# Optimization experiments

Hardware: AMD Instinct MI355X
Metric: run time of the kernel (lower is better)

The kernel has to match this reference:

```python
import jax, jax.numpy as jnp
import numpy as np

B = 32; NPG = 500; N = B * NPG; E = 256000; F = 1024; OD = 128
DD = 80; TD = 32; NH = 4; DH = TD // NH; DFF = 128; NL = 2
LSUB = 128; MAXLEN = 4 * LSUB
NEG = -1e9; SLOPE = 0.01; EPS = 1e-5


def setup_inputs() -> dict:
    key = jax.random.key(0)
    ks = iter(jax.random.split(key, 64))
    nrm = lambda *s: jax.random.normal(next(ks), s, jnp.float32)
    w = lambda *s: nrm(*s) * 0.02
    inp = {}
    inp["pro1_x"] = nrm(N, F)
    inp["pro2_x"] = nrm(N, F)
    inp["pro1_edge_index"] = jax.random.randint(next(ks), (2, E), 0, N)
    inp["pro2_edge_index"] = jax.random.randint(next(ks), (2, E), 0, N)
    inp["pro1_batch"] = jnp.repeat(jnp.arange(B), NPG)
    inp["pro2_batch"] = jnp.repeat(jnp.arange(B), NPG)
    for nm in ("mas1_straight", "mas1_flipped", "mas2_straight", "mas2_flipped"):
        inp[nm] = nrm(B, LSUB, DD)
        inp[nm + "_lengths"] = jax.random.randint(next(ks), (B,), 1, LSUB + 1)
    inp["gcn1_w"] = w(F, F); inp["gcn1_b"] = jnp.zeros(F)
    inp["gcn2_w"] = w(F, F); inp["gcn2_b"] = jnp.zeros(F)
    inp["fc1_w"] = w(OD, F); inp["fc1_b"] = jnp.zeros(OD)
    inp["fc2_w"] = w(OD, F); inp["fc2_b"] = jnp.zeros(OD)
    inp["red_w"] = w(TD - 2, DD); inp["red_b"] = jnp.zeros(TD - 2)
    inp["attn_in_w"] = w(NL, 3 * TD, TD); inp["attn_in_b"] = jnp.zeros((NL, 3 * TD))
    inp["attn_out_w"] = w(NL, TD, TD); inp["attn_out_b"] = jnp.zeros((NL, TD))
    inp["ln1_w"] = jnp.ones((NL, TD)); inp["ln1_b"] = jnp.zeros((NL, TD))
    inp["ln2_w"] = jnp.ones((NL, TD)); inp["ln2_b"] = jnp.zeros((NL, TD))
    inp["ff1_w"] = w(NL, DFF, TD); inp["ff1_b"] = jnp.zeros((NL, DFF))
    inp["ff2_w"] = w(NL, TD, DFF); inp["ff2_b"] = jnp.zeros((NL, TD))
    inp["final_w"] = w(1, 2 * OD + TD); inp["final_b"] = jnp.zeros(1)
    return inp


def _leaky(v):
    return jnp.where(v >= 0, v, SLOPE * v)


def _gcn(x, ei, W, b):
    # GCNConv: x' = D^-1/2 (A + I) D^-1/2 (x @ W^T) + b
    sl = jnp.arange(N, dtype=ei.dtype)
    src = jnp.concatenate([ei[0], sl])
    dst = jnp.concatenate([ei[1], sl])
    deg = jax.ops.segment_sum(jnp.ones(src.shape[0], x.dtype), dst, N)
    dinv = jax.lax.rsqrt(deg)
    norm = (dinv[src] * dinv[dst])[:, None]
    h = x @ W.T
    return jax.ops.segment_sum(h[src] * norm, dst, N) + b


def _gmp(x, batch):
    # global mean pool per graph
    s = jax.ops.segment_sum(x, batch, B)
    c = jax.ops.segment_sum(jnp.ones(x.shape[0], x.dtype), batch, B)
    return s / c[:, None]


def _ln(x, w, b):
    m = x.mean(-1, keepdims=True)
    v = ((x - m) ** 2).mean(-1, keepdims=True)
    return (x - m) * jax.lax.rsqrt(v + EPS) * w + b


def _forward(pro1_x, pro1_edge_index, pro1_batch, pro2_x, pro2_edge_index, pro2_batch,
             mas1_straight, mas1_flipped, mas2_straight, mas2_flipped,
             mas1_straight_lengths, mas1_flipped_lengths, mas2_straight_lengths, mas2_flipped_lengths,
             gcn1_w, gcn1_b, fc1_w, fc1_b, gcn2_w, gcn2_b, fc2_w, fc2_b,
             red_w, red_b, attn_in_w, attn_in_b, attn_out_w, attn_out_b,
             ln1_w, ln1_b, ln2_w, ln2_b, ff1_w, ff1_b, ff2_w, ff2_b,
             final_w, final_b):
    # --- graph branches (dropout = identity at inference) ---
    x1 = _leaky(_gcn(pro1_x, pro1_edge_index, gcn1_w, gcn1_b))
    x1 = _leaky(_gmp(x1, pro1_batch) @ fc1_w.T + fc1_b)           # [B, OD]
    x2 = _leaky(_gcn(pro2_x, pro2_edge_index, gcn2_w, gcn2_b))
    x2 = _leaky(_gmp(x2, pro2_batch) @ fc2_w.T + fc2_b)           # [B, OD]

    # --- vectorized ragged pack: project, append indicators, scatter to offsets ---
    inds = ((1.0, 1.0), (0.0, 1.0), (1.0, 0.0), (0.0, 0.0))      # (straight, first)
    mas = (mas1_straight, mas1_flipped, mas2_straight, mas2_flipped)
    lens = (mas1_straight_lengths, mas1_flipped_lengths, mas2_straight_lengths, mas2_flipped_lengths)
    pos = jnp.arange(LSUB)
    brow = jnp.arange(B)[:, None]
    seq = jnp.zeros((B, MAXLEN, TD), jnp.float32)
    off = jnp.zeros((B,), lens[0].dtype)
    for m, l, (si, fi) in zip(mas, lens, inds):
        proj = m @ red_w.T + red_b                                # [B, LSUB, TD-2]
        ones = jnp.ones((B, LSUB, 1), jnp.float32)
        p = jnp.concatenate([proj, si * ones, fi * ones], -1)    # [B, LSUB, TD]
        valid = pos[None, :] < l[:, None]                        # [B, LSUB]
        idx = jnp.where(valid, off[:, None] + pos[None, :], 0)
        seq = seq.at[brow, idx].add(p * valid[..., None])
        off = off + l
    mask = jnp.arange(MAXLEN)[None, :] < off[:, None]            # [B, MAXLEN] True = valid

    # --- post-norm TransformerEncoder (relu FFN, key padding mask) ---
    x_t = seq
    for li in range(NL):
        qkv = x_t @ attn_in_w[li].T + attn_in_b[li]
        q, k, v = jnp.split(qkv, 3, axis=-1)
        q = q.reshape(B, MAXLEN, NH, DH)
        k = k.reshape(B, MAXLEN, NH, DH)
        v = v.reshape(B, MAXLEN, NH, DH)
        scores = jnp.einsum('bqhd,bkhd->bhqk', q, k) / np.float32(np.sqrt(DH))
        scores = jnp.where(mask[:, None, None, :], scores, NEG)
        attn = jax.nn.softmax(scores, axis=-1)
        o = jnp.einsum('bhqk,bkhd->bqhd', attn, v).reshape(B, MAXLEN, TD)
        o = o @ attn_out_w[li].T + attn_out_b[li]
        x_t = _ln(x_t + o, ln1_w[li], ln1_b[li])
        h = jax.nn.relu(x_t @ ff1_w[li].T + ff1_b[li]) @ ff2_w[li].T + ff2_b[li]
        x_t = _ln(x_t + h, ln2_w[li], ln2_b[li])

    mf = mask[..., None].astype(jnp.float32)
    mas_out = (x_t * mf).sum(1) / mf.sum(1)                      # masked mean [B, TD]

    combined = jnp.concatenate([x1, x2, mas_out], axis=1)        # [B, 2*OD + TD]
    return combined @ final_w.T + final_b                        # [B, 1]


def reference(pro1_x, pro1_edge_index, pro1_batch, pro2_x, pro2_edge_index, pro2_batch,
              mas1_straight, mas1_flipped, mas2_straight, mas2_flipped,
              mas1_straight_lengths, mas1_flipped_lengths, mas2_straight_lengths, mas2_flipped_lengths,
              gcn1_w, gcn1_b, fc1_w, fc1_b, gcn2_w, gcn2_b, fc2_w, fc2_b,
              red_w, red_b, attn_in_w, attn_in_b, attn_out_w, attn_out_b,
              ln1_w, ln1_b, ln2_w, ln2_b, ff1_w, ff1_b, ff2_w, ff2_b,
              final_w, final_b):
    return _forward(pro1_x, pro1_edge_index, pro1_batch, pro2_x, pro2_edge_index, pro2_batch,
                    mas1_straight, mas1_flipped, mas2_straight, mas2_flipped,
                    mas1_straight_lengths, mas1_flipped_lengths, mas2_straight_lengths, mas2_flipped_lengths,
                    gcn1_w, gcn1_b, fc1_w, fc1_b, gcn2_w, gcn2_b, fc2_w, fc2_b,
                    red_w, red_b, attn_in_w, attn_in_b, attn_out_w, attn_out_b,
                    ln1_w, ln1_b, ln2_w, ln2_b, ff1_w, ff1_b, ff2_w, ff2_b,
                    final_w, final_b)
```

## Files before the change

### kernel.cpp

```cpp
#include <hip/hip_runtime.h>
#include <stdint.h>

#define N_NODES 16000
#define MPAD_   16128
#define B_      32
#define NPG_    500
#define E_      256000
#define F_      1024
#define OD_     128
#define DD_     80
#define TD_     32
#define NH_     4
#define DH_     8
#define DFF_    128
#define LSUB_   128
#define MAXLEN_ 512
#define EPS_    1e-5f
#define SLOPE_  0.01f

typedef __bf16 bf16x8 __attribute__((ext_vector_type(8)));
typedef float  f32x4  __attribute__((ext_vector_type(4)));

__device__ __forceinline__ float leaky(float v) { return v >= 0.f ? v : SLOPE_ * v; }

__device__ __forceinline__ unsigned short f2bf(float f) {
  unsigned u = __float_as_uint(f);
  u += 0x7FFFu + ((u >> 16) & 1u);
  return (unsigned short)(u >> 16);
}
__device__ __forceinline__ float bf2f(unsigned short u) {
  return __uint_as_float((unsigned)u << 16);
}

__device__ __forceinline__ void gld_lds16(const void* g, void* l) {
  __builtin_amdgcn_global_load_lds(
      (const __attribute__((address_space(1))) unsigned int*)g,
      (__attribute__((address_space(3))) unsigned int*)l, 16, 0, 0);
}

__global__ void k_f2bf2(const float* __restrict__ in0, const float* __restrict__ in1,
                        unsigned short* __restrict__ out0, unsigned short* __restrict__ out1,
                        int n4) {
  const float* in = blockIdx.y ? in1 : in0;
  unsigned short* out = blockIdx.y ? out1 : out0;
  int i = blockIdx.x * blockDim.x + threadIdx.x;
  int stride = gridDim.x * blockDim.x;
  for (; i < n4; i += stride) {
    float4 v = ((const float4*)in)[i];
    ushort4 o;
    o.x = f2bf(v.x); o.y = f2bf(v.y); o.z = f2bf(v.z); o.w = f2bf(v.w);
    ((ushort4*)out)[i] = o;
  }
}

#define LDSA(bf, ks, row) (*(const bf16x8*)&lds[(bf)*16384 + (ks)*8192 + (row)*32 + rs])
#define LDSB(bf, ks, row) (*(const bf16x8*)&lds[32768 + (bf)*16384 + (ks)*8192 + (row)*32 + rs])
#define STG_A(bf, R, kti) do { \
  gld_lds16(&Ag[(size_t)(mBase + (R) + r4) * 1024 + (kti) * 64 + c4],      &lds[(bf)*16384 + (R)*32 + t*8]); \
  gld_lds16(&Ag[(size_t)(mBase + (R) + r4) * 1024 + (kti) * 64 + 32 + c4], &lds[(bf)*16384 + 8192 + (R)*32 + t*8]); \
} while (0)
#define STG_B(bf, R, kti) do { \
  gld_lds16(&Bg[(size_t)(nBase + (R) + r4) * 1024 + (kti) * 64 + c4],      &lds[32768 + (bf)*16384 + (R)*32 + t*8]); \
  gld_lds16(&Bg[(size_t)(nBase + (R) + r4) * 1024 + (kti) * 64 + 32 + c4], &lds[32768 + (bf)*16384 + 8192 + (R)*32 + t*8]); \
} while (0)
#define RD_Q0(bf) do { \
  _Pragma("unroll") for (int mi = 0; mi < 4; ++mi) \
  _Pragma("unroll") for (int ks = 0; ks < 2; ++ks) \
    aLo[mi][ks] = LDSA(bf, ks, wrow * 128 + mi * 16 + l15); \
  _Pragma("unroll") for (int ni = 0; ni < 2; ++ni) \
  _Pragma("unroll") for (int ks = 0; ks < 2; ++ks) \
    bLo[ni][ks] = LDSB(bf, ks, wcol * 64 + ni * 16 + l15); \
} while (0)
#define RD_BHI(bf) do { \
  _Pragma("unroll") for (int ni = 0; ni < 2; ++ni) \
  _Pragma("unroll") for (int ks = 0; ks < 2; ++ks) \
    bHi[ni][ks] = LDSB(bf, ks, wcol * 64 + (2 + ni) * 16 + l15); \
} while (0)
#define RD_AHI(bf) do { \
  _Pragma("unroll") for (int mi = 0; mi < 4; ++mi) \
  _Pragma("unroll") for (int ks = 0; ks < 2; ++ks) \
    aHi[mi][ks] = LDSA(bf, ks, wrow * 128 + (4 + mi) * 16 + l15); \
} while (0)
#define MM_Q0() do { __builtin_amdgcn_s_setprio(1); \
  _Pragma("unroll") for (int mi = 0; mi < 4; ++mi) \
  _Pragma("unroll") for (int ni = 0; ni < 2; ++ni) \
  _Pragma("unroll") for (int ks = 0; ks < 2; ++ks) \
    acc[mi][ni] = __builtin_amdgcn_mfma_f32_16x16x32_bf16(aLo[mi][ks], bLo[ni][ks], acc[mi][ni], 0, 0, 0); \
  __builtin_amdgcn_s_setprio(0); } while (0)
#define MM_Q1() do { __builtin_amdgcn_s_setprio(1); \
  _Pragma("unroll") for (int mi = 0; mi < 4; ++mi) \
  _Pragma("unroll") for (int ni = 0; ni < 2; ++ni) \
  _Pragma("unroll") for (int ks = 0; ks < 2; ++ks) \
    acc[mi][2 + ni] = __builtin_amdgcn_mfma_f32_16x16x32_bf16(aLo[mi][ks], bHi[ni][ks], acc[mi][2 + ni], 0, 0, 0); \
  __builtin_amdgcn_s_setprio(0); } while (0)
#define MM_Q3() do { __builtin_amdgcn_s_setprio(1); \
  _Pragma("unroll") for (int mi = 0; mi < 4; ++mi) \
  _Pragma("unroll") for (int ni = 0; ni < 2; ++ni) \
  _Pragma("unroll") for (int ks = 0; ks < 2; ++ks) \
    acc[4 + mi][2 + ni] = __builtin_amdgcn_mfma_f32_16x16x32_bf16(aHi[mi][ks], bHi[ni][ks], acc[4 + mi][2 + ni], 0, 0, 0); \
  __builtin_amdgcn_s_setprio(0); } while (0)
#define MM_Q2() do { __builtin_amdgcn_s_setprio(1); \
  _Pragma("unroll") for (int mi = 0; mi < 4; ++mi) \
  _Pragma("unroll") for (int ni = 0; ni < 2; ++ni) \
  _Pragma("unroll") for (int ks = 0; ks < 2; ++ks) \
    acc[4 + mi][ni] = __builtin_amdgcn_mfma_f32_16x16x32_bf16(aHi[mi][ks], bLo[ni][ks], acc[4 + mi][ni], 0, 0, 0); \
  __builtin_amdgcn_s_setprio(0); } while (0)
#define BAR() do { __builtin_amdgcn_sched_barrier(0); __builtin_amdgcn_s_barrier(); \
                   __builtin_amdgcn_sched_barrier(0); } while (0)
#define LGKM0() do { asm volatile("s_waitcnt lgkmcnt(0)" ::: "memory"); \
                     __builtin_amdgcn_sched_barrier(0); } while (0)
#define VM4() do { asm volatile("s_waitcnt vmcnt(4)" ::: "memory"); } while (0)
#define VM0() do { asm volatile("s_waitcnt vmcnt(0)" ::: "memory"); } while (0)

__global__ __launch_bounds__(512, 2) void k_gemm256(const unsigned short* __restrict__ Ag,
                                                    const unsigned short* __restrict__ Bg,
                                                    unsigned short* __restrict__ Cg) {
  __shared__ short lds[65536];
  const int j  = blockIdx.x;
  const int x8 = j & 7;
  const int chunk = (x8 < 4) ? x8 * 32 : 128 + (x8 - 4) * 31;
  const int pos = chunk + (j >> 3);
  const int mb = pos >> 2, nb = pos & 3;
  const size_t g = blockIdx.z;
  Ag += g * (size_t)MPAD_ * 1024;
  Bg += g * (size_t)1024 * 1024;
  Cg += g * (size_t)MPAD_ * 1024;
  const int t = threadIdx.x;
  const int lane = t & 63, wave = t >> 6;
  const int wrow = wave >> 2, wcol = wave & 3;
  const int quad = lane >> 4, l15 = lane & 15;
  const int mBase = mb * 256, nBase = nb * 256;
  const int r4 = t >> 2;
  const int c4 = (((t & 3) - ((t >> 3) & 3)) & 3) * 8;
  const int rs = ((quad + (l15 >> 1)) & 3) * 8;

  f32x4 acc[8][4];
  f32x4 zero = {0.f, 0.f, 0.f, 0.f};
#pragma unroll
  for (int i = 0; i < 8; ++i)
#pragma unroll
    for (int jn = 0; jn < 4; ++jn) acc[i][jn] = zero;

  bf16x8 aLo[4][2], aHi[4][2], bLo[2][2], bHi[2][2];

  STG_A(0, 0, 0); STG_A(0, 128, 0); STG_B(0, 0, 0); STG_B(0, 128, 0);
  STG_B(1, 0, 1); STG_B(1, 128, 1);
  VM4();
  BAR();

  for (int kt = 0; kt < 16; kt += 2) {
    const bool s2 = (kt + 2) < 16;
    const bool s3 = (kt + 3) < 16;
    RD_Q0(0);
    STG_A(1, 0, kt + 1);
    BAR(); LGKM0(); MM_Q0(); BAR();
    RD_BHI(0);
    STG_A(1, 128, kt + 1);
    BAR(); LGKM0(); MM_Q1(); BAR();
    RD_AHI(0);
    if (s2) STG_B(0, 0, kt + 2);
    BAR(); LGKM0(); MM_Q3(); BAR();
    if (s2) { STG_B(0, 128, kt + 2); VM4(); } else VM0();
    BAR(); MM_Q2(); BAR();
    RD_Q0(1);
    if (s2) STG_A(0, 0, kt + 2);
    BAR(); LGKM0(); MM_Q0(); BAR();
    RD_BHI(1);
    if (s2) STG_A(0, 128, kt + 2);
    BAR(); LGKM0(); MM_Q1(); BAR();
    RD_AHI(1);
    if (s3) STG_B(1, 0, kt + 3);
    BAR(); LGKM0(); MM_Q3(); BAR();
    if (s3) { STG_B(1, 128, kt + 3); VM4(); }
    BAR(); MM_Q2(); BAR();
  }

#pragma unroll
  for (int mi = 0; mi < 8; ++mi)
#pragma unroll
    for (int ni = 0; ni < 4; ++ni)
#pragma unroll
      for (int r = 0; r < 4; ++r) {
        int grow = mBase + wrow * 128 + mi * 16 + quad * 4 + r;
        int gcol = nBase + wcol * 64 + ni * 16 + l15;
        Cg[(size_t)grow * 1024 + gcol] = f2bf(acc[mi][ni][r]);
      }
}

__global__ void k_hist(const int* __restrict__ ei0, const int* __restrict__ ei1,
                       int* __restrict__ cnt, int e, int n) {
  const int g = blockIdx.y;
  const int* dst = (g ? ei1 : ei0) + e;
  int i = blockIdx.x * 256 + threadIdx.x;
  if (i < e) atomicAdd(&cnt[g * n + dst[i]], 1);
}

__global__ void k_scan(const int* __restrict__ cnt_all, int* __restrict__ rowstart_all,
                       int* __restrict__ cursor_all, float* __restrict__ dinv_all, int n) {
  const int g = blockIdx.x;
  const int* cnt = cnt_all + g * n;
  int* rowstart = rowstart_all + g * (n + 1);
  int* cursor   = cursor_all + g * n;
  float* dinv   = dinv_all + g * n;
  __shared__ int part[256];
  __shared__ int base[257];
  int t = threadIdx.x;
  int chunk = (n + 255) >> 8;
  int s = 0;
  for (int j = 0; j < chunk; ++j) {
    int idx = t * chunk + j;
    if (idx < n) s += cnt[idx];
  }
  part[t] = s;
  __syncthreads();
  if (t == 0) {
    int a = 0;
    for (int i = 0; i < 256; ++i) { base[i] = a; a += part[i]; }
    base[256] = a;
  }
  __syncthreads();
  int a = base[t];
  for (int j = 0; j < chunk; ++j) {
    int idx = t * chunk + j;
    if (idx < n) {
      int c = cnt[idx];
      rowstart[idx] = a; cursor[idx] = a; a += c;
      dinv[idx] = rsqrtf((float)c + 1.0f);
    }
  }
  if (t == 0) rowstart[n] = base[256];
}

__global__ void k_scatter(const int* __restrict__ ei0, const int* __restrict__ ei1,
                          const float* __restrict__ dinv_all, int* __restrict__ cursor_all,
                          int* __restrict__ csr_all, float* __restrict__ csrw_all,
                          int e, int n) {
  const int g = blockIdx.y;
  const int* ei = g ? ei1 : ei0;
  int i = blockIdx.x * 256 + threadIdx.x;
  if (i < e) {
    int s = ei[i], d = ei[e + i];
    int p = atomicAdd(&cursor_all[g * n + d], 1);
    csr_all[(size_t)g * e + p]  = s;
    csrw_all[(size_t)g * e + p] = dinv_all[g * n + s] * dinv_all[g * n + d];
  }
}

__global__ __launch_bounds__(64) void k_gather(const ushort2* __restrict__ h2,
                                               const float* __restrict__ dinv,
                                               const int* __restrict__ rowstart,
                                               const int* __restrict__ csr,
                                               const float* __restrict__ csrw,
                                               ushort2* __restrict__ agg2) {
  const int sl = blockIdx.x;
  const int i  = blockIdx.y;
  const int t  = threadIdx.x;
  __shared__ int   ssrc[64];
  __shared__ float sw[64];
  const float di = dinv[i];
  const size_t fo = (size_t)sl * 64 + t;
  ushort2 sv = h2[(size_t)i * 512 + fo];
  const float selfw = di * di;
  float ax = bf2f(sv.x) * selfw, ay = bf2f(sv.y) * selfw;
  const int beg = rowstart[i], end = rowstart[i + 1];
  for (int base = beg; base < end; base += 64) {
    int c = end - base; if (c > 64) c = 64;
    __syncthreads();
    if (t < c) { ssrc[t] = csr[base + t]; sw[t] = csrw[base + t]; }
    __syncthreads();
    int j = 0;
    for (; j + 4 <= c; j += 4) {
      ushort2 v0 = h2[(size_t)ssrc[j]     * 512 + fo];
      ushort2 v1 = h2[(size_t)ssrc[j + 1] * 512 + fo];
      ushort2 v2 = h2[(size_t)ssrc[j + 2] * 512 + fo];
      ushort2 v3 = h2[(size_t)ssrc[j + 3] * 512 + fo];
      float w0 = sw[j], w1 = sw[j + 1], w2 = sw[j + 2], w3 = sw[j + 3];
      ax += bf2f(v0.x) * w0 + bf2f(v1.x) * w1 + bf2f(v2.x) * w2 + bf2f(v3.x) * w3;
      ay += bf2f(v0.y) * w0 + bf2f(v1.y) * w1 + bf2f(v2.y) * w2 + bf2f(v3.y) * w3;
    }
    for (; j < c; ++j) {
      ushort2 v0 = h2[(size_t)ssrc[j] * 512 + fo];
      float w0 = sw[j];
      ax += bf2f(v0.x) * w0; ay += bf2f(v0.y) * w0;
    }
  }
  ushort2 o; o.x = f2bf(ax); o.y = f2bf(ay);
  agg2[(size_t)i * 512 + fo] = o;
}

__global__ void k_pool(const unsigned short* __restrict__ agg_all,
                       const float* __restrict__ bias0, const float* __restrict__ bias1,
                       float* __restrict__ pooled_all) {
  int f = blockIdx.x * 256 + threadIdx.x;
  int z = blockIdx.z;
  int g = z >> 5, b = z & 31;
  const unsigned short* agg = agg_all + (size_t)g * N_NODES * F_;
  const float* bias = g ? bias1 : bias0;
  float* pooled = pooled_all + (size_t)g * B_ * F_;
  int r0 = blockIdx.y * 100;
  float bf = bias[f];
  float s = 0.f;
  for (int r = 0; r < 100; ++r)
    s += leaky(bf2f(agg[(size_t)(b * NPG_ + r0 + r) * F_ + f]) + bf);
  atomicAdd(&pooled[b * F_ + f], s);
}

__global__ void k_fc(const float* __restrict__ pooled_all,
                     const float* __restrict__ w0, const float* __restrict__ w1,
                     const float* __restrict__ bias0, const float* __restrict__ bias1,
                     float* __restrict__ out0, float* __restrict__ out1) {
  int b = blockIdx.x, o = threadIdx.x, g = blockIdx.y;
  const float* p  = pooled_all + (size_t)g * B_ * F_ + b * F_;
  const float* wr = (g ? w1 : w0) + o * F_;
  const float* bias = g ? bias1 : bias0;
  float* out = g ? out1 : out0;
  float acc = 0.f;
  for (int f = 0; f < F_; ++f) acc += p[f] * wr[f];
  out[b * OD_ + o] = leaky(acc * (1.f / 500.f) + bias[o]);
}

__global__ void k_pack(const float* __restrict__ m0, const float* __restrict__ m1,
                       const float* __restrict__ m2, const float* __restrict__ m3,
                       const int* __restrict__ l0, const int* __restrict__ l1,
                       const int* __restrict__ l2, const int* __restrict__ l3,
                       const float* __restrict__ rw, const float* __restrict__ rb,
                       float* __restrict__ seq) {
  __shared__ float xs[DD_];
  const int p = blockIdx.x, b = blockIdx.y, k = blockIdx.z;
  const float* mas = (k == 0) ? m0 : (k == 1) ? m1 : (k == 2) ? m2 : m3;
  const int*   lk  = (k == 0) ? l0 : (k == 1) ? l1 : (k == 2) ? l2 : l3;
  const int len = lk[b];
  if (p >= len) return;
  int off = 0;
  if (k > 0) off += l0[b];
  if (k > 1) off += l1[b];
  if (k > 2) off += l2[b];
  const int t = threadIdx.x;
  for (int d = t; d < DD_; d += 64) xs[d] = mas[(size_t)(b * LSUB_ + p) * DD_ + d];
  __syncthreads();
  if (t < TD_) {
    float v;
    if (t < TD_ - 2) {
      float a = rb[t];
      const float* w = &rw[t * DD_];
      for (int d = 0; d < DD_; ++d) a += xs[d] * w[d];
      v = a;
    } else if (t == TD_ - 2) {
      v = (k == 0 || k == 2) ? 1.f : 0.f;
    } else {
      v = (k < 2) ? 1.f : 0.f;
    }
    seq[((size_t)b * MAXLEN_ + off + p) * TD_ + t] = v;
  }
}

__global__ void k_totlen(const int* __restrict__ l0, const int* __restrict__ l1,
                         const int* __restrict__ l2, const int* __restrict__ l3,
                         int* __restrict__ tot) {
  int b = threadIdx.x;
  if (b < B_) tot[b] = l0[b] + l1[b] + l2[b] + l3[b];
}

__global__ void k_qkv(const float* __restrict__ xt, const float* __restrict__ w,
                      const float* __restrict__ bias, const int* __restrict__ tot,
                      float* __restrict__ qkv) {
  __shared__ float xs[TD_];
  const int row = blockIdx.x;
  if ((row & (MAXLEN_ - 1)) >= tot[row >> 9]) return;
  const int t = threadIdx.x;
  if (t < TD_) xs[t] = xt[(size_t)row * TD_ + t];
  __syncthreads();
  if (t < 3 * TD_) {
    float a = bias[t];
    const float* wr = &w[t * TD_];
#pragma unroll
    for (int k = 0; k < TD_; ++k) a += xs[k] * wr[k];
    qkv[(size_t)row * 96 + t] = a;
  }
}

__global__ __launch_bounds__(128) void k_attn(const float* __restrict__ qkv,
                                              const int* __restrict__ tot,
                                              float* __restrict__ obuf) {
  __shared__ float Kl[MAXLEN_ * DH_];
  __shared__ float Vl[MAXLEN_ * DH_];
  const int h = blockIdx.x, b = blockIdx.y, qz = blockIdx.z;
  const int t = threadIdx.x;
  const int L = tot[b];
  if (qz * 64 >= L) return;
  const float* base = &qkv[(size_t)b * MAXLEN_ * 96];
  for (int i = t; i < L * DH_; i += 128) {
    int p = i >> 3, d = i & 7;
    Kl[i] = base[p * 96 + 32 + h * 8 + d];
    Vl[i] = base[p * 96 + 64 + h * 8 + d];
  }
  __syncthreads();
  const int qi = qz * 64 + (t >> 1);
  if (qi >= L) return;
  const int half = t & 1;
  const float scale = 0.35355339059327373f;
  float q[8];
#pragma unroll
  for (int d = 0; d < 8; ++d) q[d] = base[qi * 96 + h * 8 + d] * scale;

  float l0 = 0.f, l1 = 0.f;
  float a0[8] = {0, 0, 0, 0, 0, 0, 0, 0};
  float a1[8] = {0, 0, 0, 0, 0, 0, 0, 0};
  int j = half;
  for (; j + 2 < L; j += 4) {
    const float* kr0 = &Kl[j * 8];
    const float* kr1 = &Kl[(j + 2) * 8];
    float s0 = 0.f, s1 = 0.f;
#pragma unroll
    for (int d = 0; d < 8; ++d) { s0 += q[d] * kr0[d]; s1 += q[d] * kr1[d]; }
    float p0 = __expf(s0), p1 = __expf(s1);
    l0 += p0; l1 += p1;
    const float* vr0 = &Vl[j * 8];
    const float* vr1 = &Vl[(j + 2) * 8];
#pragma unroll
    for (int d = 0; d < 8; ++d) { a0[d] += p0 * vr0[d]; a1[d] += p1 * vr1[d]; }
  }
  for (; j < L; j += 2) {
    const float* kr = &Kl[j * 8];
    float s = 0.f;
#pragma unroll
    for (int d = 0; d < 8; ++d) s += q[d] * kr[d];
    float p = __expf(s);
    l0 += p;
    const float* vr = &Vl[j * 8];
#pragma unroll
    for (int d = 0; d < 8; ++d) a0[d] += p * vr[d];
  }
  float l = l0 + l1;
#pragma unroll
  for (int d = 0; d < 8; ++d) a0[d] += a1[d];
  l += __shfl_xor(l, 1);
#pragma unroll
  for (int d = 0; d < 8; ++d) a0[d] += __shfl_xor(a0[d], 1);
  float inv = 1.f / l;
  const int dbase = half * 4;
  float4 o;
  o.x = a0[dbase + 0] * inv; o.y = a0[dbase + 1] * inv;
  o.z = a0[dbase + 2] * inv; o.w = a0[dbase + 3] * inv;
  *(float4*)&obuf[((size_t)b * MAXLEN_ + qi) * TD_ + h * 8 + dbase] = o;
}

__global__ void k_oproj_ln(const float* __restrict__ obuf, const float* __restrict__ w,
                           const float* __restrict__ bias, const float* __restrict__ lw,
                           const float* __restrict__ lb, const int* __restrict__ tot,
                           float* __restrict__ xt) {
  const int t = threadIdx.x;
  const int r = blockIdx.x * 8 + (t >> 5);
  if ((r & (MAXLEN_ - 1)) >= tot[r >> 9]) return;
  const int j = t & 31;
  const float* orow = &obuf[(size_t)r * TD_];
  float a = bias[j] + xt[(size_t)r * TD_ + j];
  const float* wr = &w[j * TD_];
#pragma unroll
  for (int k = 0; k < TD_; ++k) a += orow[k] * wr[k];
  float s1 = a, s2 = a * a;
#pragma unroll
  for (int m = 1; m < 32; m <<= 1) {
    s1 += __shfl_xor(s1, m, 32);
    s2 += __shfl_xor(s2, m, 32);
  }
  float mean = s1 * (1.f / 32.f);
  float var  = s2 * (1.f / 32.f) - mean * mean;
  xt[(size_t)r * TD_ + j] = (a - mean) * rsqrtf(var + EPS_) * lw[j] + lb[j];
}

__global__ void k_ffn_ln(const float* __restrict__ w1, const float* __restrict__ b1,
                         const float* __restrict__ w2, const float* __restrict__ b2,
                         const float* __restrict__ lw, const float* __restrict__ lb,
                         const int* __restrict__ tot, float* __restrict__ xt) {
  const int r = blockIdx.x, t = threadIdx.x;
  if ((r & (MAXLEN_ - 1)) >= tot[r >> 9]) return;
  __shared__ float xs[TD_];
  __shared__ float hb[DFF_];
  if (t < TD_) xs[t] = xt[(size_t)r * TD_ + t];
  __syncthreads();
  {
    float a = b1[t];
    const float* wr = &w1[t * TD_];
#pragma unroll
    for (int k = 0; k < TD_; ++k) a += xs[k] * wr[k];
    hb[t] = fmaxf(a, 0.f);
  }
  __syncthreads();
  if (t < TD_) {
    float a = b2[t] + xs[t];
    const float* wr = &w2[t * DFF_];
#pragma unroll
    for (int k = 0; k < DFF_; ++k) a += hb[k] * wr[k];
    float s1 = a, s2 = a * a;
#pragma unroll
    for (int m = 1; m < 32; m <<= 1) {
      s1 += __shfl_xor(s1, m, 32);
      s2 += __shfl_xor(s2, m, 32);
    }
    float mean = s1 * (1.f / 32.f);
    float var  = s2 * (1.f / 32.f) - mean * mean;
    xt[(size_t)r * TD_ + t] = (a - mean) * rsqrtf(var + EPS_) * lw[t] + lb[t];
  }
}

__global__ void k_maskmean(const float* __restrict__ xt, const int* __restrict__ tot,
                           float* __restrict__ mout) {
  __shared__ float sbuf[8][32];
  const int b = blockIdx.x, t = threadIdx.x;
  const int j = t & 31, c = t >> 5;
  const int L = tot[b];
  float s = 0.f;
  for (int p = c; p < L; p += 8) s += xt[((size_t)b * MAXLEN_ + p) * TD_ + j];
  sbuf[c][j] = s;
  __syncthreads();
  if (t < 32) {
    float a = 0.f;
#pragma unroll
    for (int cc = 0; cc < 8; ++cc) a += sbuf[cc][t];
    mout[b * TD_ + t] = a / (float)L;
  }
}

__global__ void k_final(const float* __restrict__ x1, const float* __restrict__ x2,
                        const float* __restrict__ mo, const float* __restrict__ fw,
                        const float* __restrict__ fb, float* __restrict__ out) {
  const int b = blockIdx.x, t = threadIdx.x;
  float s = 0.f;
  for (int i = t; i < 2 * OD_ + TD_; i += 64) {
    float c = (i < OD_) ? x1[b * OD_ + i]
            : (i < 2 * OD_) ? x2[b * OD_ + (i - OD_)]
            : mo[b * TD_ + (i - 2 * OD_)];
    s += fw[i] * c;
  }
#pragma unroll
  for (int m = 1; m < 64; m <<= 1) s += __shfl_xor(s, m, 64);
  if (t == 0) out[b] = s + fb[0];
}

extern "C" void kernel_launch(void* const* d_in, const int* in_sizes, int n_in,
                              void* d_out, int out_size, void* d_ws, size_t ws_size,
                              hipStream_t stream) {
  (void)in_sizes; (void)n_in; (void)out_size; (void)ws_size;
  const float* pro_x[2]  = {(const float*)d_in[0], (const float*)d_in[1]};
  const int*   pro_ei[2] = {(const int*)d_in[2], (const int*)d_in[3]};
  const float* mas[4]    = {(const float*)d_in[6], (const float*)d_in[8],
                            (const float*)d_in[10], (const float*)d_in[12]};
  const int*   lens[4]   = {(const int*)d_in[7], (const int*)d_in[9],
                            (const int*)d_in[11], (const int*)d_in[13]};
  const float* gw[2]  = {(const float*)d_in[14], (const float*)d_in[16]};
  const float* gb[2]  = {(const float*)d_in[15], (const float*)d_in[17]};
  const float* fcw[2] = {(const float*)d_in[18], (const float*)d_in[20]};
  const float* fcb[2] = {(const float*)d_in[19], (const float*)d_in[21]};
  const float* red_w = (const float*)d_in[22];
  const float* red_b = (const float*)d_in[23];
  const float* attn_in_w  = (const float*)d_in[24];
  const float* attn_in_b  = (const float*)d_in[25];
  const float* attn_out_w = (const float*)d_in[26];
  const float* attn_out_b = (const float*)d_in[27];
  const float* ln1_w = (const float*)d_in[28];
  const float* ln1_b = (const float*)d_in[29];
  const float* ln2_w = (const float*)d_in[30];
  const float* ln2_b = (const float*)d_in[31];
  const float* ff1_w = (const float*)d_in[32];
  const float* ff1_b = (const float*)d_in[33];
  const float* ff2_w = (const float*)d_in[34];
  const float* ff2_b = (const float*)d_in[35];
  const float* final_w = (const float*)d_in[36];
  const float* final_b = (const float*)d_in[37];
  float* out = (float*)d_out;

  char* p = (char*)d_ws;
  auto carve = [&](size_t bytes) -> void* {
    void* r = (void*)p;
    p += (bytes + 255) & ~(size_t)255;
    return r;
  };
  unsigned short* xb  = (unsigned short*)carve((size_t)2 * MPAD_ * F_ * 2);
  unsigned short* Wb  = (unsigned short*)carve((size_t)2 * F_ * F_ * 2);
  unsigned short* h   = (unsigned short*)carve((size_t)2 * MPAD_ * F_ * 2);
  unsigned short* agg = (unsigned short*)carve((size_t)2 * N_NODES * F_ * 2);
  int*   cnt      = (int*)carve((size_t)2 * N_NODES * 4);
  float* dinv     = (float*)carve((size_t)2 * N_NODES * 4);
  int*   rowstart = (int*)carve((size_t)2 * (N_NODES + 1) * 4);
  int*   cursor   = (int*)carve((size_t)2 * N_NODES * 4);
  int*   csr      = (int*)carve((size_t)2 * E_ * 4);
  float* csrw     = (float*)carve((size_t)2 * E_ * 4);
  float* pooled   = (float*)carve((size_t)2 * B_ * F_ * 4);
  float* xg[2];
  xg[0] = (float*)carve((size_t)B_ * OD_ * 4);
  xg[1] = (float*)carve((size_t)B_ * OD_ * 4);
  float* seq    = (float*)carve((size_t)B_ * MAXLEN_ * TD_ * 4);
  float* qkv    = (float*)carve((size_t)B_ * MAXLEN_ * 96 * 4);
  float* obuf   = (float*)carve((size_t)B_ * MAXLEN_ * TD_ * 4);
  int*   totlen = (int*)carve((size_t)B_ * 4);
  float* masout = (float*)carve((size_t)B_ * TD_ * 4);

  k_f2bf2<<<dim3(1024, 2), 256, 0, stream>>>(pro_x[0], pro_x[1], xb,
                                             xb + (size_t)MPAD_ * F_, (N_NODES * F_) / 4);
  k_f2bf2<<<dim3(512, 2), 256, 0, stream>>>(gw[0], gw[1], Wb, Wb + (size_t)F_ * F_,
                                            (F_ * F_) / 4);
  k_gemm256<<<dim3(252, 1, 2), 512, 0, stream>>>(xb, Wb, h);
  hipMemsetAsync(cnt, 0, (size_t)2 * N_NODES * 4, stream);
  k_hist<<<dim3(1000, 2), 256, 0, stream>>>(pro_ei[0], pro_ei[1], cnt, E_, N_NODES);
  k_scan<<<2, 256, 0, stream>>>(cnt, rowstart, cursor, dinv, N_NODES);
  k_scatter<<<dim3(1000, 2), 256, 0, stream>>>(pro_ei[0], pro_ei[1], dinv, cursor,
                                               csr, csrw, E_, N_NODES);
  for (int g = 0; g < 2; ++g) {
    k_gather<<<dim3(8, N_NODES), 64, 0, stream>>>(
        (const ushort2*)(h + (size_t)g * MPAD_ * F_), dinv + (size_t)g * N_NODES,
        rowstart + (size_t)g * (N_NODES + 1), csr + (size_t)g * E_, csrw + (size_t)g * E_,
        (ushort2*)(agg + (size_t)g * N_NODES * F_));
  }
  hipMemsetAsync(pooled, 0, (size_t)2 * B_ * F_ * 4, stream);
  k_pool<<<dim3(4, 5, 64), 256, 0, stream>>>(agg, gb[0], gb[1], pooled);
  k_fc<<<dim3(B_, 2), 128, 0, stream>>>(pooled, fcw[0], fcw[1], fcb[0], fcb[1],
                                        xg[0], xg[1]);

  hipMemsetAsync(seq, 0, (size_t)B_ * MAXLEN_ * TD_ * 4, stream);
  k_pack<<<dim3(LSUB_, B_, 4), 64, 0, stream>>>(mas[0], mas[1], mas[2], mas[3],
                                                lens[0], lens[1], lens[2], lens[3],
                                                red_w, red_b, seq);
  k_totlen<<<1, 64, 0, stream>>>(lens[0], lens[1], lens[2], lens[3], totlen);

  for (int li = 0; li < 2; ++li) {
    k_qkv<<<B_ * MAXLEN_, 128, 0, stream>>>(seq, attn_in_w + (size_t)li * 96 * TD_,
                                            attn_in_b + (size_t)li * 96, totlen, qkv);
    k_attn<<<dim3(NH_, B_, 8), 128, 0, stream>>>(qkv, totlen, obuf);
    k_oproj_ln<<<(B_ * MAXLEN_) / 8, 256, 0, stream>>>(
        obuf, attn_out_w + (size_t)li * TD_ * TD_, attn_out_b + (size_t)li * TD_,
        ln1_w + (size_t)li * TD_, ln1_b + (size_t)li * TD_, totlen, seq);
    k_ffn_ln<<<B_ * MAXLEN_, 128, 0, stream>>>(
        ff1_w + (size_t)li * DFF_ * TD_, ff1_b + (size_t)li * DFF_,
        ff2_w + (size_t)li * TD_ * DFF_, ff2_b + (size_t)li * TD_,
        ln2_w + (size_t)li * TD_, ln2_b + (size_t)li * TD_, totlen, seq);
  }

  k_maskmean<<<B_, 256, 0, stream>>>(seq, totlen, masout);
  k_final<<<B_, 64, 0, stream>>>(xg[0], xg[1], masout, final_w, final_b, out);
}
```

Measured before the change: 782.9 us.

## Merge GCN gathers, fuse post-attention and final kernels, coalesce FC

The two per-graph edge-gather launches become one grid with four nodes per block. Each wave now reads CSR indices and weights straight from global memory instead of staging them in shared memory behind barriers. The FC kernel caches the pooled row in shared memory, and each wave computes output rows with coalesced weight reads and a shuffle reduction. The out-projection+LayerNorm and FFN+LayerNorm kernels are fused into one per-row kernel, mask-mean and the final dot product are fused, and the memset of the sequence buffer is dropped. This cuts launches, barriers and intermediate memory round trips, but it relies on padded sequence rows never being read uninitialised.

```diff
diff --git a/kernel.cpp b/kernel.cpp
--- a/kernel.cpp
+++ b/kernel.cpp
@@ -246,43 +246,44 @@
   }
 }
 
-__global__ __launch_bounds__(64) void k_gather(const ushort2* __restrict__ h2,
-                                               const float* __restrict__ dinv,
-                                               const int* __restrict__ rowstart,
-                                               const int* __restrict__ csr,
-                                               const float* __restrict__ csrw,
-                                               ushort2* __restrict__ agg2) {
+__global__ __launch_bounds__(256) void k_gather(const ushort2* __restrict__ h2_all,
+                                                const float* __restrict__ dinv_all,
+                                                const int* __restrict__ rowstart_all,
+                                                const int* __restrict__ csr_all,
+                                                const float* __restrict__ csrw_all,
+                                                ushort2* __restrict__ agg2_all) {
+  const int g = blockIdx.z;
+  const ushort2* h2 = h2_all + (size_t)g * MPAD_ * 512;
+  const float* dinv = dinv_all + (size_t)g * N_NODES;
+  const int* rowstart = rowstart_all + (size_t)g * (N_NODES + 1);
+  const int* csr = csr_all + (size_t)g * E_;
+  const float* csrw = csrw_all + (size_t)g * E_;
+  ushort2* agg2 = agg2_all + (size_t)g * N_NODES * 512;
   const int sl = blockIdx.x;
-  const int i  = blockIdx.y;
-  const int t  = threadIdx.x;
-  __shared__ int   ssrc[64];
-  __shared__ float sw[64];
+  const int i  = blockIdx.y * 4 + (threadIdx.x >> 6);
+  const int lane = threadIdx.x & 63;
+  const size_t fo = (size_t)sl * 64 + lane;
   const float di = dinv[i];
-  const size_t fo = (size_t)sl * 64 + t;
   ushort2 sv = h2[(size_t)i * 512 + fo];
   const float selfw = di * di;
   float ax = bf2f(sv.x) * selfw, ay = bf2f(sv.y) * selfw;
   const int beg = rowstart[i], end = rowstart[i + 1];
-  for (int base = beg; base < end; base += 64) {
-    int c = end - base; if (c > 64) c = 64;
-    __syncthreads();
-    if (t < c) { ssrc[t] = csr[base + t]; sw[t] = csrw[base + t]; }
-    __syncthreads();
-    int j = 0;
-    for (; j + 4 <= c; j += 4) {
-      ushort2 v0 = h2[(size_t)ssrc[j]     * 512 + fo];
-      ushort2 v1 = h2[(size_t)ssrc[j + 1] * 512 + fo];
-      ushort2 v2 = h2[(size_t)ssrc[j + 2] * 512 + fo];
-      ushort2 v3 = h2[(size_t)ssrc[j + 3] * 512 + fo];
-      float w0 = sw[j], w1 = sw[j + 1], w2 = sw[j + 2], w3 = sw[j + 3];
-      ax += bf2f(v0.x) * w0 + bf2f(v1.x) * w1 + bf2f(v2.x) * w2 + bf2f(v3.x) * w3;
-      ay += bf2f(v0.y) * w0 + bf2f(v1.y) * w1 + bf2f(v2.y) * w2 + bf2f(v3.y) * w3;
-    }
-    for (; j < c; ++j) {
-      ushort2 v0 = h2[(size_t)ssrc[j] * 512 + fo];
-      float w0 = sw[j];
-      ax += bf2f(v0.x) * w0; ay += bf2f(v0.y) * w0;
-    }
+  int j = beg;
+  for (; j + 4 <= end; j += 4) {
+    int s0 = csr[j], s1 = csr[j + 1], s2 = csr[j + 2], s3 = csr[j + 3];
+    float w0 = csrw[j], w1 = csrw[j + 1], w2 = csrw[j + 2], w3 = csrw[j + 3];
+    ushort2 v0 = h2[(size_t)s0 * 512 + fo];
+    ushort2 v1 = h2[(size_t)s1 * 512 + fo];
+    ushort2 v2 = h2[(size_t)s2 * 512 + fo];
+    ushort2 v3 = h2[(size_t)s3 * 512 + fo];
+    ax += bf2f(v0.x) * w0 + bf2f(v1.x) * w1 + bf2f(v2.x) * w2 + bf2f(v3.x) * w3;
+    ay += bf2f(v0.y) * w0 + bf2f(v1.y) * w1 + bf2f(v2.y) * w2 + bf2f(v3.y) * w3;
+  }
+  for (; j < end; ++j) {
+    int s0 = csr[j];
+    float w0 = csrw[j];
+    ushort2 v0 = h2[(size_t)s0 * 512 + fo];
+    ax += bf2f(v0.x) * w0; ay += bf2f(v0.y) * w0;
   }
   ushort2 o; o.x = f2bf(ax); o.y = f2bf(ay);
   agg2[(size_t)i * 512 + fo] = o;
@@ -305,18 +306,29 @@
   atomicAdd(&pooled[b * F_ + f], s);
 }
 
-__global__ void k_fc(const float* __restrict__ pooled_all,
+__global__ __launch_bounds__(256) void k_fc(const float* __restrict__ pooled_all,
                      const float* __restrict__ w0, const float* __restrict__ w1,
                      const float* __restrict__ bias0, const float* __restrict__ bias1,
                      float* __restrict__ out0, float* __restrict__ out1) {
-  int b = blockIdx.x, o = threadIdx.x, g = blockIdx.y;
-  const float* p  = pooled_all + (size_t)g * B_ * F_ + b * F_;
-  const float* wr = (g ? w1 : w0) + o * F_;
+  __shared__ float ps[F_];
+  const int b = blockIdx.x, g = blockIdx.y, t = threadIdx.x;
+  const float* p = pooled_all + (size_t)g * B_ * F_ + b * F_;
+  const float* w = g ? w1 : w0;
   const float* bias = g ? bias1 : bias0;
   float* out = g ? out1 : out0;
-  float acc = 0.f;
-  for (int f = 0; f < F_; ++f) acc += p[f] * wr[f];
-  out[b * OD_ + o] = leaky(acc * (1.f / 500.f) + bias[o]);
+  ((float4*)ps)[t] = ((const float4*)p)[t];
+  __syncthreads();
+  const int wave = t >> 6, lane = t & 63;
+  for (int oo = 0; oo < 32; ++oo) {
+    const int o = wave * 32 + oo;
+    const float* wr = w + (size_t)o * F_;
+    float a = 0.f;
+#pragma unroll
+    for (int c = 0; c < 16; ++c) a += wr[c * 64 + lane] * ps[c * 64 + lane];
+#pragma unroll
+    for (int m = 1; m < 64; m <<= 1) a += __shfl_xor(a, m, 64);
+    if (lane == 0) out[b * OD_ + o] = leaky(a * (1.f / 500.f) + bias[o]);
+  }
 }
 
 __global__ void k_pack(const float* __restrict__ m0, const float* __restrict__ m1,
@@ -445,53 +457,29 @@
   *(float4*)&obuf[((size_t)b * MAXLEN_ + qi) * TD_ + h * 8 + dbase] = o;
 }
 
-__global__ void k_oproj_ln(const float* __restrict__ obuf, const float* __restrict__ w,
-                           const float* __restrict__ bias, const float* __restrict__ lw,
-                           const float* __restrict__ lb, const int* __restrict__ tot,
-                           float* __restrict__ xt) {
-  const int t = threadIdx.x;
-  const int r = blockIdx.x * 8 + (t >> 5);
-  if ((r & (MAXLEN_ - 1)) >= tot[r >> 9]) return;
-  const int j = t & 31;
-  const float* orow = &obuf[(size_t)r * TD_];
-  float a = bias[j] + xt[(size_t)r * TD_ + j];
-  const float* wr = &w[j * TD_];
-#pragma unroll
-  for (int k = 0; k < TD_; ++k) a += orow[k] * wr[k];
-  float s1 = a, s2 = a * a;
-#pragma unroll
-  for (int m = 1; m < 32; m <<= 1) {
-    s1 += __shfl_xor(s1, m, 32);
-    s2 += __shfl_xor(s2, m, 32);
-  }
-  float mean = s1 * (1.f / 32.f);
-  float var  = s2 * (1.f / 32.f) - mean * mean;
-  xt[(size_t)r * TD_ + j] = (a - mean) * rsqrtf(var + EPS_) * lw[j] + lb[j];
-}
-
-__global__ void k_ffn_ln(const float* __restrict__ w1, const float* __restrict__ b1,
-                         const float* __restrict__ w2, const float* __restrict__ b2,
-                         const float* __restrict__ lw, const float* __restrict__ lb,
-                         const int* __restrict__ tot, float* __restrict__ xt) {
+__global__ __launch_bounds__(128) void k_post(const float* __restrict__ obuf,
+                                              const float* __restrict__ ow,
+                                              const float* __restrict__ ob,
+                                              const float* __restrict__ l1w,
+                                              const float* __restrict__ l1b,
+                                              const float* __restrict__ f1w,
+                                              const float* __restrict__ f1b,
+                                              const float* __restrict__ f2w,
+                                              const float* __restrict__ f2b,
+                                              const float* __restrict__ l2w,
+                                              const float* __restrict__ l2b,
+                                              const int* __restrict__ tot,
+                                              float* __restrict__ xt) {
   const int r = blockIdx.x, t = threadIdx.x;
   if ((r & (MAXLEN_ - 1)) >= tot[r >> 9]) return;
   __shared__ float xs[TD_];
   __shared__ float hb[DFF_];
-  if (t < TD_) xs[t] = xt[(size_t)r * TD_ + t];
-  __syncthreads();
-  {
-    float a = b1[t];
-    const float* wr = &w1[t * TD_];
-#pragma unroll
-    for (int k = 0; k < TD_; ++k) a += xs[k] * wr[k];
-    hb[t] = fmaxf(a, 0.f);
-  }
-  __syncthreads();
   if (t < TD_) {
-    float a = b2[t] + xs[t];
-    const float* wr = &w2[t * DFF_];
-#pragma unroll
-    for (int k = 0; k < DFF_; ++k) a += hb[k] * wr[k];
+    const float* orow = &obuf[(size_t)r * TD_];
+    float a = ob[t] + xt[(size_t)r * TD_ + t];
+    const float* wr = &ow[t * TD_];
+#pragma unroll
+    for (int k = 0; k < TD_; ++k) a += orow[k] * wr[k];
     float s1 = a, s2 = a * a;
 #pragma unroll
     for (int m = 1; m < 32; m <<= 1) {
@@ -500,13 +488,43 @@
     }
     float mean = s1 * (1.f / 32.f);
     float var  = s2 * (1.f / 32.f) - mean * mean;
-    xt[(size_t)r * TD_ + t] = (a - mean) * rsqrtf(var + EPS_) * lw[t] + lb[t];
-  }
-}
-
-__global__ void k_maskmean(const float* __restrict__ xt, const int* __restrict__ tot,
-                           float* __restrict__ mout) {
+    xs[t] = (a - mean) * rsqrtf(var + EPS_) * l1w[t] + l1b[t];
+  }
+  __syncthreads();
+  {
+    float a = f1b[t];
+    const float* wr = &f1w[t * TD_];
+#pragma unroll
+    for (int k = 0; k < TD_; ++k) a += xs[k] * wr[k];
+    hb[t] = fmaxf(a, 0.f);
+  }
+  __syncthreads();
+  if (t < TD_) {
+    float a = f2b[t] + xs[t];
+    const float* wr = &f2w[t * DFF_];
+#pragma unroll
+    for (int k = 0; k < DFF_; ++k) a += hb[k] * wr[k];
+    float s1 = a, s2 = a * a;
+#pragma unroll
+    for (int m = 1; m < 32; m <<= 1) {
+      s1 += __shfl_xor(s1, m, 32);
+      s2 += __shfl_xor(s2, m, 32);
+    }
+    float mean = s1 * (1.f / 32.f);
+    float var  = s2 * (1.f / 32.f) - mean * mean;
+    xt[(size_t)r * TD_ + t] = (a - mean) * rsqrtf(var + EPS_) * l2w[t] + l2b[t];
+  }
+}
+
+__global__ __launch_bounds__(256) void k_maskfinal(const float* __restrict__ xt,
+                                                   const int* __restrict__ tot,
+                                                   const float* __restrict__ x1,
+                                                   const float* __restrict__ x2,
+                                                   const float* __restrict__ fw,
+                                                   const float* __restrict__ fb,
+                                                   float* __restrict__ out) {
   __shared__ float sbuf[8][32];
+  __shared__ float mo[TD_];
   const int b = blockIdx.x, t = threadIdx.x;
   const int j = t & 31, c = t >> 5;
   const int L = tot[b];
@@ -518,24 +536,21 @@
     float a = 0.f;
 #pragma unroll
     for (int cc = 0; cc < 8; ++cc) a += sbuf[cc][t];
-    mout[b * TD_ + t] = a / (float)L;
-  }
-}
-
-__global__ void k_final(const float* __restrict__ x1, const float* __restrict__ x2,
-                        const float* __restrict__ mo, const float* __restrict__ fw,
-                        const float* __restrict__ fb, float* __restrict__ out) {
-  const int b = blockIdx.x, t = threadIdx.x;
-  float s = 0.f;
-  for (int i = t; i < 2 * OD_ + TD_; i += 64) {
-    float c = (i < OD_) ? x1[b * OD_ + i]
-            : (i < 2 * OD_) ? x2[b * OD_ + (i - OD_)]
-            : mo[b * TD_ + (i - 2 * OD_)];
-    s += fw[i] * c;
-  }
-#pragma unroll
-  for (int m = 1; m < 64; m <<= 1) s += __shfl_xor(s, m, 64);
-  if (t == 0) out[b] = s + fb[0];
+    mo[t] = a / (float)L;
+  }
+  __syncthreads();
+  if (t < 64) {
+    float s2 = 0.f;
+    for (int i = t; i < 2 * OD_ + TD_; i += 64) {
+      float cv = (i < OD_) ? x1[b * OD_ + i]
+               : (i < 2 * OD_) ? x2[b * OD_ + (i - OD_)]
+               : mo[i - 2 * OD_];
+      s2 += fw[i] * cv;
+    }
+#pragma unroll
+    for (int m = 1; m < 64; m <<= 1) s2 += __shfl_xor(s2, m, 64);
+    if (t == 0) out[b] = s2 + fb[0];
+  }
 }
 
 extern "C" void kernel_launch(void* const* d_in, const int* in_sizes, int n_in,
@@ -594,7 +609,6 @@
   float* qkv    = (float*)carve((size_t)B_ * MAXLEN_ * 96 * 4);
   float* obuf   = (float*)carve((size_t)B_ * MAXLEN_ * TD_ * 4);
   int*   totlen = (int*)carve((size_t)B_ * 4);
-  float* masout = (float*)carve((size_t)B_ * TD_ * 4);
 
   k_f2bf2<<<dim3(1024, 2), 256, 0, stream>>>(pro_x[0], pro_x[1], xb,
                                              xb + (size_t)MPAD_ * F_, (N_NODES * F_) / 4);
@@ -606,18 +620,13 @@
   k_scan<<<2, 256, 0, stream>>>(cnt, rowstart, cursor, dinv, N_NODES);
   k_scatter<<<dim3(1000, 2), 256, 0, stream>>>(pro_ei[0], pro_ei[1], dinv, cursor,
                                                csr, csrw, E_, N_NODES);
-  for (int g = 0; g < 2; ++g) {
-    k_gather<<<dim3(8, N_NODES), 64, 0, stream>>>(
-        (const ushort2*)(h + (size_t)g * MPAD_ * F_), dinv + (size_t)g * N_NODES,
-        rowstart + (size_t)g * (N_NODES + 1), csr + (size_t)g * E_, csrw + (size_t)g * E_,
-        (ushort2*)(agg + (size_t)g * N_NODES * F_));
-  }
+  k_gather<<<dim3(8, 4000, 2), 256, 0, stream>>>((const ushort2*)h, dinv, rowstart,
+                                                 csr, csrw, (ushort2*)agg);
   hipMemsetAsync(pooled, 0, (size_t)2 * B_ * F_ * 4, stream);
   k_pool<<<dim3(4, 5, 64), 256, 0, stream>>>(agg, gb[0], gb[1], pooled);
-  k_fc<<<dim3(B_, 2), 128, 0, stream>>>(pooled, fcw[0], fcw[1], fcb[0], fcb[1],
+  k_fc<<<dim3(B_, 2), 256, 0, stream>>>(pooled, fcw[0], fcw[1], fcb[0], fcb[1],
                                         xg[0], xg[1]);
 
-  hipMemsetAsync(seq, 0, (size_t)B_ * MAXLEN_ * TD_ * 4, stream);
   k_pack<<<dim3(LSUB_, B_, 4), 64, 0, stream>>>(mas[0], mas[1], mas[2], mas[3],
                                                 lens[0], lens[1], lens[2], lens[3],
                                                 red_w, red_b, seq);
@@ -627,15 +636,13 @@
     k_qkv<<<B_ * MAXLEN_, 128, 0, stream>>>(seq, attn_in_w + (size_t)li * 96 * TD_,
                                             attn_in_b + (size_t)li * 96, totlen, qkv);
     k_attn<<<dim3(NH_, B_, 8), 128, 0, stream>>>(qkv, totlen, obuf);
-    k_oproj_ln<<<(B_ * MAXLEN_) / 8, 256, 0, stream>>>(
+    k_post<<<B_ * MAXLEN_, 128, 0, stream>>>(
         obuf, attn_out_w + (size_t)li * TD_ * TD_, attn_out_b + (size_t)li * TD_,
-        ln1_w + (size_t)li * TD_, ln1_b + (size_t)li * TD_, totlen, seq);
-    k_ffn_ln<<<B_ * MAXLEN_, 128, 0, stream>>>(
+        ln1_w + (size_t)li * TD_, ln1_b + (size_t)li * TD_,
         ff1_w + (size_t)li * DFF_ * TD_, ff1_b + (size_t)li * DFF_,
         ff2_w + (size_t)li * TD_ * DFF_, ff2_b + (size_t)li * TD_,
         ln2_w + (size_t)li * TD_, ln2_b + (size_t)li * TD_, totlen, seq);
   }
 
-  k_maskmean<<<B_, 256, 0, stream>>>(seq, totlen, masout);
-  k_final<<<B_, 64, 0, stream>>>(xg[0], xg[1], masout, final_w, final_b, out);
-}
+  k_maskfinal<<<B_, 256, 0, stream>>>(seq, totlen, xg[0], xg[1], final_w, final_b, out);
+}
```

Measured after the change: 793.3 us. Within noise of the previous version (+1.3%).
